# Performance work log

Measured on AMD Instinct MI355X. Metric: run time of the kernel, lower is better.

The kernel has to match this reference:

```python
import jax, jax.numpy as jnp
import numpy as np

H = 4096       # hidden_size
NH = 32        # query heads
NKV = 2        # kv heads (multi_query_group_num)
HD = H // NH   # 128 head_dim
ROT = HD // 2  # GLM style: rotary applied to first half of head_dim
BASE = 10000.0
B, S = 2, 2048


def setup_inputs() -> dict:
    key = jax.random.key(0)
    k0, k1, k2, k3 = jax.random.split(key, 4)
    hidden_states = jax.random.normal(k0, (B, S, H), jnp.float32) * 0.02
    w_qkv = jax.random.normal(k1, (H, (NH + 2 * NKV) * HD), jnp.float32) * 0.02
    b_qkv = jax.random.normal(k2, ((NH + 2 * NKV) * HD,), jnp.float32) * 0.02
    w_dense = jax.random.normal(k3, (NH * HD, H), jnp.float32) * 0.02
    positions = jnp.broadcast_to(jnp.arange(S, dtype=jnp.int32), (B, S))
    return {"hidden_states": hidden_states, "w_qkv": w_qkv, "b_qkv": b_qkv,
            "w_dense": w_dense, "positions": positions}


def _glm_rope(x, positions):
    # x: [B, S, nheads, HD]; rotate first ROT dims, interleaved (non-neox) pairs
    inv_freq = 1.0 / (BASE ** (jnp.arange(0, ROT, 2, dtype=jnp.float32) / ROT))  # [ROT/2]
    ang = positions.astype(jnp.float32)[..., None] * inv_freq                     # [B,S,ROT/2]
    cos = jnp.cos(ang)[:, :, None, :]
    sin = jnp.sin(ang)[:, :, None, :]
    xr, xp = x[..., :ROT], x[..., ROT:]
    x1, x2 = xr[..., 0::2], xr[..., 1::2]
    o1 = x1 * cos - x2 * sin
    o2 = x1 * sin + x2 * cos
    rot = jnp.stack([o1, o2], axis=-1).reshape(xr.shape)
    return jnp.concatenate([rot, xp], axis=-1)


def reference(hidden_states, w_qkv, b_qkv, w_dense, positions):
    qkv = hidden_states @ w_qkv + b_qkv                       # [B,S,4608]
    q, k, v = jnp.split(qkv, [NH * HD, NH * HD + NKV * HD], axis=-1)
    q = q.reshape(B, S, NH, HD)
    k = k.reshape(B, S, NKV, HD)
    v = v.reshape(B, S, NKV, HD)
    q = _glm_rope(q, positions)
    k = _glm_rope(k, positions)
    # GQA: group query heads per kv head
    G = NH // NKV
    q = q.reshape(B, S, NKV, G, HD)
    scale = HD ** -0.5
    scores = jnp.einsum('bsgqd,btgd->bgqst', q, k) * scale    # [B,NKV,G,S,S]
    causal = jnp.tril(jnp.ones((S, S), dtype=bool))
    scores = jnp.where(causal, scores, jnp.finfo(scores.dtype).min)
    probs = jax.nn.softmax(scores, axis=-1)
    out = jnp.einsum('bgqst,btgd->bsgqd', probs, v)           # [B,S,NKV,G,HD]
    out = out.reshape(B, S, NH * HD)
    return out @ w_dense                                      # [B,S,H]
```

## Files before the change

kernel.cpp:

```cpp
#include <hip/hip_runtime.h>
#include <math.h>

#define B_    2
#define S_    2048
#define H_    4096
#define NH_   32
#define NKV_  2
#define HD_   128
#define ROT_  64
#define NQKV_ 4608
#define M_    4096
#define SCALE_ 0.088388347648318447f

typedef __attribute__((ext_vector_type(8))) short s16x8;
typedef __attribute__((ext_vector_type(4))) float f32x4;

__device__ __forceinline__ unsigned short f2bf(float x) {
  union { float f; unsigned u; } v; v.f = x;
  unsigned r = (v.u + 0x7fffu + ((v.u >> 16) & 1u)) >> 16;
  return (unsigned short)r;
}
__device__ __forceinline__ float bf2f(unsigned short u) {
  union { unsigned u; float f; } v; v.u = ((unsigned)u) << 16;
  return v.f;
}
__device__ __forceinline__ void gl_lds16(const unsigned short* g, unsigned short* l) {
  __builtin_amdgcn_global_load_lds(
      (const __attribute__((address_space(1))) void*)g,
      (__attribute__((address_space(3))) void*)l, 16, 0, 0);
}

__global__ __launch_bounds__(256) void cvt_bf16_kernel(
    const float* __restrict__ in, unsigned short* __restrict__ o, long n)
{
  long i = ((long)blockIdx.x * blockDim.x + threadIdx.x) * 8;
  if (i >= n) return;
  float4 a = *(const float4*)(in + i);
  float4 b = *(const float4*)(in + i + 4);
  s16x8 v;
  v[0] = f2bf(a.x); v[1] = f2bf(a.y); v[2] = f2bf(a.z); v[3] = f2bf(a.w);
  v[4] = f2bf(b.x); v[5] = f2bf(b.y); v[6] = f2bf(b.z); v[7] = f2bf(b.w);
  *(s16x8*)(o + i) = v;
}

__global__ __launch_bounds__(256) void wtrans_kernel(
    const float* __restrict__ w, unsigned short* __restrict__ wt, int K, int N)
{
  __shared__ __align__(16) unsigned short T[64][72];
  const int tid = threadIdx.x;
  const int k0 = blockIdx.x * 64;
  const int n0 = blockIdx.y * 64;

#pragma unroll
  for (int i = 0; i < 4; ++i) {
    int idx = tid + i * 256;
    int kr = idx >> 4;
    int nc = (idx & 15) << 2;
    float4 v = *(const float4*)(w + (size_t)(k0 + kr) * N + n0 + nc);
    T[nc + 0][kr] = f2bf(v.x);
    T[nc + 1][kr] = f2bf(v.y);
    T[nc + 2][kr] = f2bf(v.z);
    T[nc + 3][kr] = f2bf(v.w);
  }
  __syncthreads();
#pragma unroll
  for (int i = 0; i < 2; ++i) {
    int idx = tid + i * 256;
    int nr = idx >> 3;
    int kc = (idx & 7) << 3;
    s16x8 v = *(const s16x8*)&T[nr][kc];
    *(s16x8*)&wt[(size_t)(n0 + nr) * K + k0 + kc] = v;
  }
}

template<bool BF16OUT>
__global__ __launch_bounds__(256) void gemm_bf16_kernel(
    const unsigned short* __restrict__ A, const unsigned short* __restrict__ Bt,
    const float* __restrict__ bias, void* __restrict__ Cv,
    int M, int N, int K)
{
  __shared__ __align__(16) unsigned short As[128 * 32];
  __shared__ __align__(16) unsigned short Bs[128 * 32];
  const int tid  = threadIdx.x;
  const int lane = tid & 63;
  const int w    = tid >> 6;
  const int quad = lane >> 4;
  const int l15  = lane & 15;
  const int wm   = w >> 1;
  const int wn   = w & 1;
  const int bm = blockIdx.y * 128;
  const int bn = blockIdx.x * 128;

  const int r16 = lane >> 2;
  const int kc  = (lane & 3) << 3;
  const int c0  = w * 2;
  const unsigned short* Ag0 = A  + (size_t)(bm + (c0 + 0) * 16 + r16) * K + kc;
  const unsigned short* Ag1 = A  + (size_t)(bm + (c0 + 1) * 16 + r16) * K + kc;
  const unsigned short* Bg0 = Bt + (size_t)(bn + (c0 + 0) * 16 + r16) * K + kc;
  const unsigned short* Bg1 = Bt + (size_t)(bn + (c0 + 1) * 16 + r16) * K + kc;
  unsigned short* As0 = &As[(c0 + 0) * 512];
  unsigned short* As1 = &As[(c0 + 1) * 512];
  unsigned short* Bs0 = &Bs[(c0 + 0) * 512];
  unsigned short* Bs1 = &Bs[(c0 + 1) * 512];

  const unsigned short* Af = &As[(wm * 64 + l15) * 32 + (quad << 3)];
  const unsigned short* Bf = &Bs[(wn * 64 + l15) * 32 + (quad << 3)];

  f32x4 acc[4][4];
#pragma unroll
  for (int i = 0; i < 4; ++i)
#pragma unroll
    for (int j = 0; j < 4; ++j)
#pragma unroll
      for (int e = 0; e < 4; ++e) acc[i][j][e] = 0.0f;

  for (int k0 = 0; k0 < K; k0 += 32) {
    gl_lds16(Ag0 + k0, As0);
    gl_lds16(Ag1 + k0, As1);
    gl_lds16(Bg0 + k0, Bs0);
    gl_lds16(Bg1 + k0, Bs1);
    __syncthreads();
    s16x8 af[4], bfr[4];
#pragma unroll
    for (int mi = 0; mi < 4; ++mi) af[mi]  = *(const s16x8*)(Af + mi * 512);
#pragma unroll
    for (int ni = 0; ni < 4; ++ni) bfr[ni] = *(const s16x8*)(Bf + ni * 512);
#pragma unroll
    for (int mi = 0; mi < 4; ++mi)
#pragma unroll
      for (int ni = 0; ni < 4; ++ni)
        acc[mi][ni] = __builtin_amdgcn_mfma_f32_16x16x32_bf16(
            af[mi], bfr[ni], acc[mi][ni], 0, 0, 0);
    __syncthreads();
  }

  float bv[4];
#pragma unroll
  for (int ni = 0; ni < 4; ++ni)
    bv[ni] = bias ? bias[bn + wn * 64 + ni * 16 + l15] : 0.0f;

#pragma unroll
  for (int mi = 0; mi < 4; ++mi)
#pragma unroll
    for (int i = 0; i < 4; ++i) {
      size_t row = (size_t)(bm + wm * 64 + mi * 16 + (quad << 2) + i);
#pragma unroll
      for (int ni = 0; ni < 4; ++ni) {
        size_t idx = row * N + bn + wn * 64 + ni * 16 + l15;
        float val = acc[mi][ni][i] + bv[ni];
        if (BF16OUT) ((unsigned short*)Cv)[idx] = f2bf(val);
        else         ((float*)Cv)[idx] = val;
      }
    }
}

__global__ __launch_bounds__(256) void rope_kernel(
    unsigned short* __restrict__ qkv, const int* __restrict__ positions)
{
  int t = blockIdx.x * blockDim.x + threadIdx.x;
  const int total = M_ * (NH_ + NKV_) * (ROT_ / 2);
  if (t >= total) return;
  int pair = t & 31;
  int hh   = (t >> 5) % (NH_ + NKV_);
  int tok  = t / (32 * (NH_ + NKV_));
  int col  = hh * HD_;
  float pos  = (float)positions[tok];
  float freq = powf(10000.0f, -(float)pair * (1.0f / 32.0f));
  float ang  = pos * freq;
  float s = sinf(ang), c = cosf(ang);
  size_t base = (size_t)tok * NQKV_ + col + 2 * pair;
  unsigned v = *(const unsigned*)(qkv + base);
  float x1 = bf2f((unsigned short)(v & 0xffffu));
  float x2 = bf2f((unsigned short)(v >> 16));
  float o1 = x1 * c - x2 * s;
  float o2 = x1 * s + x2 * c;
  *(unsigned*)(qkv + base) = (unsigned)f2bf(o1) | ((unsigned)f2bf(o2) << 16);
}

__global__ __launch_bounds__(256) void vtrans_kernel(
    const unsigned short* __restrict__ qkv, unsigned short* __restrict__ vt)
{
  __shared__ __align__(16) unsigned short T[64][72];
  const int tid = threadIdx.x;
  const int s0 = blockIdx.x * 64;
  const int c0 = blockIdx.y * 64;
  const int bg = blockIdx.z;
  const int b = bg >> 1, g = bg & 1;

#pragma unroll
  for (int i = 0; i < 2; ++i) {
    int idx = tid + i * 256;
    int sr = idx >> 3;
    int cc = (idx & 7) << 3;
    const unsigned short* p = qkv + (size_t)(b * S_ + s0 + sr) * NQKV_
                     + (NH_ + NKV_) * HD_ + g * HD_ + c0 + cc;
    s16x8 v = *(const s16x8*)p;
#pragma unroll
    for (int j = 0; j < 8; ++j) T[cc + j][sr] = (unsigned short)v[j];
  }
  __syncthreads();
#pragma unroll
  for (int i = 0; i < 2; ++i) {
    int idx = tid + i * 256;
    int cr = idx >> 3;
    int kc = idx & 7;
    s16x8 v = *(const s16x8*)&T[cr][kc << 3];
    *(s16x8*)&vt[(size_t)((bg << 7) + c0 + cr) * S_ + s0 + (kc << 3)] = v;
  }
}

#define VT_OFF 8704
#define PS_OFF 16896

__global__ __launch_bounds__(256, 2) void flash_mfma_kernel(
    const unsigned short* __restrict__ qkv, const unsigned short* __restrict__ vt,
    unsigned short* __restrict__ out)
{
  __shared__ __align__(16) unsigned short smem[26112];

  const int tid  = threadIdx.x;
  const int lane = tid & 63;
  const int w    = tid >> 6;
  const int quad = lane >> 4;
  const int l15  = lane & 15;
  const int q0 = blockIdx.x * 128;
  const int b  = blockIdx.y >> 5;
  const int h  = blockIdx.y & 31;
  const int g  = h >> 4;
  const int bg = b * NKV_ + g;
  const size_t tok0 = (size_t)b * S_;

  s16x8 qf[2][4];
#pragma unroll
  for (int mt = 0; mt < 2; ++mt) {
#pragma unroll
    for (int i = 0; i < 4; ++i) {
      int idx = tid + i * 256;
      int r = idx >> 4, c8 = (idx & 15) << 3;
      s16x8 v = *(const s16x8*)(qkv + (tok0 + q0 + mt * 64 + r) * NQKV_ + h * HD_ + c8);
      *(s16x8*)&smem[r * 136 + c8] = v;
    }
    __syncthreads();
#pragma unroll
    for (int ks = 0; ks < 4; ++ks)
      qf[mt][ks] = *(const s16x8*)&smem[(w * 16 + l15) * 136 + (quad << 3) + (ks << 5)];
    __syncthreads();
  }

  f32x4 O[2][8];
#pragma unroll
  for (int mt = 0; mt < 2; ++mt)
#pragma unroll
    for (int n = 0; n < 8; ++n)
#pragma unroll
      for (int i = 0; i < 4; ++i) O[mt][n][i] = 0.0f;
  float m_i[2][4], l_i[2][4];
#pragma unroll
  for (int mt = 0; mt < 2; ++mt)
#pragma unroll
    for (int i = 0; i < 4; ++i) { m_i[mt][i] = -INFINITY; l_i[mt][i] = 0.f; }

  const int ktend = q0 + 64;
  for (int kt = 0; kt <= ktend; kt += 64) {
#pragma unroll
    for (int i = 0; i < 4; ++i) {
      int idx = tid + i * 256;
      int key = idx >> 4, c8 = (idx & 15) << 3;
      s16x8 v = *(const s16x8*)(qkv + (tok0 + kt + key) * NQKV_ + NH_ * HD_ + g * HD_ + c8);
      *(s16x8*)&smem[key * 136 + c8] = v;
    }
#pragma unroll
    for (int i = 0; i < 4; ++i) {
      int idx = tid + i * 256;
      int c = idx >> 3, kc = idx & 7;
      s16x8 v = *(const s16x8*)&vt[(size_t)((bg << 7) + c) * S_ + kt + (kc << 3)];
      *(s16x8*)&smem[VT_OFF + (c << 6) + (((kc + c) & 7) << 3)] = v;
    }
    __syncthreads();

    f32x4 S[2][4];
#pragma unroll
    for (int mt = 0; mt < 2; ++mt)
#pragma unroll
      for (int nt = 0; nt < 4; ++nt)
#pragma unroll
        for (int i = 0; i < 4; ++i) S[mt][nt][i] = 0.0f;
#pragma unroll
    for (int nt = 0; nt < 4; ++nt) {
#pragma unroll
      for (int ks = 0; ks < 4; ++ks) {
        s16x8 kf = *(const s16x8*)&smem[(nt * 16 + l15) * 136 + (quad << 3) + (ks << 5)];
#pragma unroll
        for (int mt = 0; mt < 2; ++mt)
          S[mt][nt] = __builtin_amdgcn_mfma_f32_16x16x32_bf16(qf[mt][ks], kf, S[mt][nt], 0, 0, 0);
      }
#pragma unroll
      for (int mt = 0; mt < 2; ++mt)
#pragma unroll
        for (int i = 0; i < 4; ++i) S[mt][nt][i] *= SCALE_;
    }

#pragma unroll
    for (int mt = 0; mt < 2; ++mt) {
      if (kt >= q0 + mt * 64) {
#pragma unroll
        for (int nt = 0; nt < 4; ++nt) {
          int colG = kt + nt * 16 + l15;
#pragma unroll
          for (int i = 0; i < 4; ++i) {
            int rowG = q0 + mt * 64 + w * 16 + quad * 4 + i;
            if (colG > rowG) S[mt][nt][i] = -INFINITY;
          }
        }
      }
    }

    float alpha[2][4];
#pragma unroll
    for (int mt = 0; mt < 2; ++mt) {
      float mx[4], rs[4];
#pragma unroll
      for (int i = 0; i < 4; ++i) {
        mx[i] = fmaxf(fmaxf(S[mt][0][i], S[mt][1][i]), fmaxf(S[mt][2][i], S[mt][3][i]));
#pragma unroll
        for (int off = 1; off < 16; off <<= 1)
          mx[i] = fmaxf(mx[i], __shfl_xor(mx[i], off));
        float mn = fmaxf(m_i[mt][i], mx[i]);
        alpha[mt][i] = __expf(m_i[mt][i] - mn);
        m_i[mt][i] = mn;
        rs[i] = 0.0f;
      }
#pragma unroll
      for (int nt = 0; nt < 4; ++nt)
#pragma unroll
        for (int i = 0; i < 4; ++i) {
          float p = __expf(S[mt][nt][i] - m_i[mt][i]);
          S[mt][nt][i] = p;
          rs[i] += p;
        }
#pragma unroll
      for (int i = 0; i < 4; ++i) {
#pragma unroll
        for (int off = 1; off < 16; off <<= 1)
          rs[i] += __shfl_xor(rs[i], off);
        l_i[mt][i] = l_i[mt][i] * alpha[mt][i] + rs[i];
      }

#pragma unroll
      for (int nt = 0; nt < 4; ++nt)
#pragma unroll
        for (int i = 0; i < 4; ++i)
          smem[PS_OFF + (mt * 64 + w * 16 + quad * 4 + i) * 72 + nt * 16 + l15]
              = f2bf(S[mt][nt][i]);

#pragma unroll
      for (int n = 0; n < 8; ++n)
#pragma unroll
        for (int i = 0; i < 4; ++i) O[mt][n][i] *= alpha[mt][i];
    }

    __syncthreads();

    s16x8 pf[2][2];
#pragma unroll
    for (int mt = 0; mt < 2; ++mt)
#pragma unroll
      for (int ks2 = 0; ks2 < 2; ++ks2)
        pf[mt][ks2] = *(const s16x8*)&smem[PS_OFF + (mt * 64 + w * 16 + l15) * 72
                                           + (quad << 3) + (ks2 << 5)];
#pragma unroll
    for (int nt2 = 0; nt2 < 8; ++nt2) {
      int col = nt2 * 16 + l15;
#pragma unroll
      for (int ks2 = 0; ks2 < 2; ++ks2) {
        int kc = ks2 * 4 + quad;
        s16x8 vf = *(const s16x8*)&smem[VT_OFF + (col << 6) + (((kc + col) & 7) << 3)];
#pragma unroll
        for (int mt = 0; mt < 2; ++mt)
          O[mt][nt2] = __builtin_amdgcn_mfma_f32_16x16x32_bf16(pf[mt][ks2], vf, O[mt][nt2], 0, 0, 0);
      }
    }
    __syncthreads();
  }

#pragma unroll
  for (int mt = 0; mt < 2; ++mt) {
    float inv[4];
#pragma unroll
    for (int i = 0; i < 4; ++i) inv[i] = 1.0f / l_i[mt][i];
#pragma unroll
    for (int nt2 = 0; nt2 < 8; ++nt2)
#pragma unroll
      for (int i = 0; i < 4; ++i) {
        size_t row = tok0 + q0 + mt * 64 + w * 16 + quad * 4 + i;
        out[row * H_ + h * HD_ + nt2 * 16 + l15] = f2bf(O[mt][nt2][i] * inv[i]);
      }
  }
}

extern "C" void kernel_launch(void* const* d_in, const int* in_sizes, int n_in,
                              void* d_out, int out_size, void* d_ws, size_t ws_size,
                              hipStream_t stream)
{
  (void)in_sizes; (void)n_in; (void)out_size; (void)ws_size;
  const float* hidden    = (const float*)d_in[0];
  const float* w_qkv     = (const float*)d_in[1];
  const float* b_qkv     = (const float*)d_in[2];
  const float* w_dense   = (const float*)d_in[3];
  const int*   positions = (const int*)d_in[4];
  float* out = (float*)d_out;

  unsigned short* hbf   = (unsigned short*)d_ws;
  unsigned short* wqkvT = (unsigned short*)((char*)d_ws + 33554432);
  unsigned short* vtb   = (unsigned short*)d_ws;
  unsigned short* abf   = (unsigned short*)((char*)d_ws + 2097152);
  unsigned short* wdT   = (unsigned short*)((char*)d_ws + 35651584);
  unsigned short* qkvb  = (unsigned short*)d_out;

  cvt_bf16_kernel<<<8192, 256, 0, stream>>>(hidden, hbf, (long)M_ * H_);
  wtrans_kernel<<<dim3(H_ / 64, NQKV_ / 64), 256, 0, stream>>>(w_qkv, wqkvT, H_, NQKV_);

  gemm_bf16_kernel<true><<<dim3(NQKV_ / 128, M_ / 128), 256, 0, stream>>>(
      hbf, wqkvT, b_qkv, qkvb, M_, NQKV_, H_);

  {
    int total = M_ * (NH_ + NKV_) * (ROT_ / 2);
    rope_kernel<<<(total + 255) / 256, 256, 0, stream>>>(qkvb, positions);
  }

  vtrans_kernel<<<dim3(S_ / 64, HD_ / 64, B_ * NKV_), 256, 0, stream>>>(qkvb, vtb);
  wtrans_kernel<<<dim3(H_ / 64, H_ / 64), 256, 0, stream>>>(w_dense, wdT, H_, H_);

  flash_mfma_kernel<<<dim3(S_ / 128, B_ * NH_), 256, 0, stream>>>(qkvb, vtb, abf);

  gemm_bf16_kernel<false><<<dim3(H_ / 128, M_ / 128), 256, 0, stream>>>(
      abf, wdT, nullptr, out, M_, H_, H_);
}
```

Baseline: 922.5 us.

## Replace 128x128 GEMM with double-buffered 256x256 tile, 8-wave pipelined kernel

Both projection GEMMs move from a 128x128 single-buffered tile with 4 waves to a 256x256 tile with 8 waves and a double-buffered LDS. Global-to-LDS loads for the next K-tile are issued between MFMA phases, using explicit vmcnt waits, barriers and setprio to overlap memory with compute. The larger tile raises data reuse per load but cuts the grid to 288 and 256 blocks, which may leave compute units underused on a 256-CU part. Register use also grows from the 8x4 accumulators.

```diff
diff --git a/kernel.cpp b/kernel.cpp
--- a/kernel.cpp
+++ b/kernel.cpp
@@ -74,65 +74,106 @@
 }
 
 template<bool BF16OUT>
-__global__ __launch_bounds__(256) void gemm_bf16_kernel(
+__global__ __launch_bounds__(512, 1) void gemm256_kernel(
     const unsigned short* __restrict__ A, const unsigned short* __restrict__ Bt,
     const float* __restrict__ bias, void* __restrict__ Cv,
     int M, int N, int K)
 {
-  __shared__ __align__(16) unsigned short As[128 * 32];
-  __shared__ __align__(16) unsigned short Bs[128 * 32];
+  __shared__ __align__(16) unsigned short lds[32768];
   const int tid  = threadIdx.x;
   const int lane = tid & 63;
   const int w    = tid >> 6;
   const int quad = lane >> 4;
   const int l15  = lane & 15;
-  const int wm   = w >> 1;
-  const int wn   = w & 1;
-  const int bm = blockIdx.y * 128;
-  const int bn = blockIdx.x * 128;
-
-  const int r16 = lane >> 2;
-  const int kc  = (lane & 3) << 3;
-  const int c0  = w * 2;
-  const unsigned short* Ag0 = A  + (size_t)(bm + (c0 + 0) * 16 + r16) * K + kc;
-  const unsigned short* Ag1 = A  + (size_t)(bm + (c0 + 1) * 16 + r16) * K + kc;
-  const unsigned short* Bg0 = Bt + (size_t)(bn + (c0 + 0) * 16 + r16) * K + kc;
-  const unsigned short* Bg1 = Bt + (size_t)(bn + (c0 + 1) * 16 + r16) * K + kc;
-  unsigned short* As0 = &As[(c0 + 0) * 512];
-  unsigned short* As1 = &As[(c0 + 1) * 512];
-  unsigned short* Bs0 = &Bs[(c0 + 0) * 512];
-  unsigned short* Bs1 = &Bs[(c0 + 1) * 512];
-
-  const unsigned short* Af = &As[(wm * 64 + l15) * 32 + (quad << 3)];
-  const unsigned short* Bf = &Bs[(wn * 64 + l15) * 32 + (quad << 3)];
-
-  f32x4 acc[4][4];
-#pragma unroll
-  for (int i = 0; i < 4; ++i)
+  const int wm   = w >> 2;
+  const int wn   = w & 3;
+  const int bm = blockIdx.y * 256;
+  const int bn = blockIdx.x * 256;
+  const int NT = K >> 5;
+
+  const unsigned short* Agl = A  + (size_t)(bm + w * 32 + (lane >> 2)) * K + ((lane & 3) << 3);
+  const unsigned short* Bgl = Bt + (size_t)(bn + w * 32 + (lane >> 2)) * K + ((lane & 3) << 3);
+  const size_t j1 = (size_t)16 * K;
+
+  const int afo = (wm * 128 + l15) * 32 + (quad << 3);
+  const int bfo = (wn * 64  + l15) * 32 + (quad << 3);
+
+  f32x4 acc[8][4];
+#pragma unroll
+  for (int i = 0; i < 8; ++i)
 #pragma unroll
     for (int j = 0; j < 4; ++j)
 #pragma unroll
       for (int e = 0; e < 4; ++e) acc[i][j][e] = 0.0f;
 
-  for (int k0 = 0; k0 < K; k0 += 32) {
-    gl_lds16(Ag0 + k0, As0);
-    gl_lds16(Ag1 + k0, As1);
-    gl_lds16(Bg0 + k0, Bs0);
-    gl_lds16(Bg1 + k0, Bs1);
-    __syncthreads();
-    s16x8 af[4], bfr[4];
-#pragma unroll
-    for (int mi = 0; mi < 4; ++mi) af[mi]  = *(const s16x8*)(Af + mi * 512);
-#pragma unroll
-    for (int ni = 0; ni < 4; ++ni) bfr[ni] = *(const s16x8*)(Bf + ni * 512);
-#pragma unroll
-    for (int mi = 0; mi < 4; ++mi)
-#pragma unroll
-      for (int ni = 0; ni < 4; ++ni)
-        acc[mi][ni] = __builtin_amdgcn_mfma_f32_16x16x32_bf16(
-            af[mi], bfr[ni], acc[mi][ni], 0, 0, 0);
-    __syncthreads();
-  }
+#define STAGE_A(T, BUF) do {                                            \
+    const unsigned short* g_ = Agl + (size_t)(T) * 32;                  \
+    gl_lds16(g_,      &lds[(BUF) * 8192 + w * 1024]);                   \
+    gl_lds16(g_ + j1, &lds[(BUF) * 8192 + w * 1024 + 512]);             \
+  } while (0)
+#define STAGE_B(T, BUF) do {                                            \
+    const unsigned short* g_ = Bgl + (size_t)(T) * 32;                  \
+    gl_lds16(g_,      &lds[16384 + (BUF) * 8192 + w * 1024]);           \
+    gl_lds16(g_ + j1, &lds[16384 + (BUF) * 8192 + w * 1024 + 512]);     \
+  } while (0)
+
+  STAGE_A(0, 0);
+  STAGE_B(0, 0);
+  STAGE_A(1, 1);
+  asm volatile("s_waitcnt vmcnt(2)" ::: "memory");
+  __builtin_amdgcn_s_barrier();
+  __builtin_amdgcn_sched_barrier(0);
+
+#define TILE_BODY(CUR, TT) do {                                              \
+    const int nb_ = (CUR) ^ 1;                                               \
+                    \
+    s16x8 af[8], b0, b1;                                                     \
+    _Pragma("unroll")                                                        \
+    for (int mi = 0; mi < 8; ++mi)                                           \
+      af[mi] = *(const s16x8*)&lds[(CUR) * 8192 + afo + mi * 512];           \
+    b0 = *(const s16x8*)&lds[16384 + (CUR) * 8192 + bfo];                    \
+    b1 = *(const s16x8*)&lds[16384 + (CUR) * 8192 + bfo + 512];              \
+    { int ts_ = (TT) + 1 < NT ? (TT) + 1 : NT - 1; STAGE_B(ts_, nb_); }      \
+    __builtin_amdgcn_s_barrier();                                            \
+    __builtin_amdgcn_sched_barrier(0);                                       \
+    __builtin_amdgcn_s_setprio(1);                                           \
+    _Pragma("unroll")                                                        \
+    for (int mi = 0; mi < 8; ++mi) {                                         \
+      acc[mi][0] = __builtin_amdgcn_mfma_f32_16x16x32_bf16(af[mi], b0, acc[mi][0], 0, 0, 0); \
+      acc[mi][1] = __builtin_amdgcn_mfma_f32_16x16x32_bf16(af[mi], b1, acc[mi][1], 0, 0, 0); \
+    }                                                                        \
+    __builtin_amdgcn_s_setprio(0);                                           \
+    __builtin_amdgcn_s_barrier();                                            \
+    __builtin_amdgcn_sched_barrier(0);                                       \
+            \
+    s16x8 b2, b3;                                                            \
+    b2 = *(const s16x8*)&lds[16384 + (CUR) * 8192 + bfo + 1024];             \
+    b3 = *(const s16x8*)&lds[16384 + (CUR) * 8192 + bfo + 1536];             \
+    { int ts_ = (TT) + 2 < NT ? (TT) + 2 : NT - 1; STAGE_A(ts_, (CUR)); }    \
+    __builtin_amdgcn_s_barrier();                                            \
+    __builtin_amdgcn_sched_barrier(0);                                       \
+    __builtin_amdgcn_s_setprio(1);                                           \
+    _Pragma("unroll")                                                        \
+    for (int mi = 0; mi < 8; ++mi) {                                         \
+      acc[mi][2] = __builtin_amdgcn_mfma_f32_16x16x32_bf16(af[mi], b2, acc[mi][2], 0, 0, 0); \
+      acc[mi][3] = __builtin_amdgcn_mfma_f32_16x16x32_bf16(af[mi], b3, acc[mi][3], 0, 0, 0); \
+    }                                                                        \
+    __builtin_amdgcn_s_setprio(0);                                           \
+    asm volatile("s_waitcnt vmcnt(2)" ::: "memory");                         \
+    __builtin_amdgcn_s_barrier();                                            \
+    __builtin_amdgcn_sched_barrier(0);                                       \
+  } while (0)
+
+#pragma unroll 1
+  for (int t = 0; t < NT; t += 2) {
+    TILE_BODY(0, t);
+    TILE_BODY(1, t + 1);
+  }
+#undef TILE_BODY
+#undef STAGE_A
+#undef STAGE_B
+
+  asm volatile("s_waitcnt vmcnt(0)" ::: "memory");
 
   float bv[4];
 #pragma unroll
@@ -140,10 +181,10 @@
     bv[ni] = bias ? bias[bn + wn * 64 + ni * 16 + l15] : 0.0f;
 
 #pragma unroll
-  for (int mi = 0; mi < 4; ++mi)
+  for (int mi = 0; mi < 8; ++mi)
 #pragma unroll
     for (int i = 0; i < 4; ++i) {
-      size_t row = (size_t)(bm + wm * 64 + mi * 16 + (quad << 2) + i);
+      size_t row = (size_t)(bm + wm * 128 + mi * 16 + (quad << 2) + i);
 #pragma unroll
       for (int ni = 0; ni < 4; ++ni) {
         size_t idx = row * N + bn + wn * 64 + ni * 16 + l15;
@@ -420,7 +461,7 @@
   cvt_bf16_kernel<<<8192, 256, 0, stream>>>(hidden, hbf, (long)M_ * H_);
   wtrans_kernel<<<dim3(H_ / 64, NQKV_ / 64), 256, 0, stream>>>(w_qkv, wqkvT, H_, NQKV_);
 
-  gemm_bf16_kernel<true><<<dim3(NQKV_ / 128, M_ / 128), 256, 0, stream>>>(
+  gemm256_kernel<true><<<dim3(NQKV_ / 256, M_ / 256), 512, 0, stream>>>(
       hbf, wqkvT, b_qkv, qkvb, M_, NQKV_, H_);
 
   {
@@ -433,6 +474,6 @@
 
   flash_mfma_kernel<<<dim3(S_ / 128, B_ * NH_), 256, 0, stream>>>(qkvb, vtb, abf);
 
-  gemm_bf16_kernel<false><<<dim3(H_ / 128, M_ / 128), 256, 0, stream>>>(
+  gemm256_kernel<false><<<dim3(H_ / 256, M_ / 256), 512, 0, stream>>>(
       abf, wdT, nullptr, out, M_, H_, H_);
 }
```

After: 847.4 us. 1.09x faster.
